# Kernel optimization log

Measured on AMD Instinct MI355X. Metric: run time of the kernel, lower is better.

Reference implementation:

```python
import jax, jax.numpy as jnp
import numpy as np

B, S, D, H = 2, 2048, 1024, 16
DK = D // H


def setup_inputs() -> dict:
    key = jax.random.key(0)
    ks = jax.random.split(key, 12)
    std = 1.0 / np.sqrt(D)
    inp = {
        "query": jax.random.normal(ks[0], (B, S, D), jnp.float32),
        "key": jax.random.normal(ks[1], (B, S, D), jnp.float32),
        "value": jax.random.normal(ks[2], (B, S, D), jnp.float32),
        # causal decoder mask [B, 1, S, S]; 0 -> masked
        "mask": jnp.broadcast_to(jnp.tril(jnp.ones((S, S), jnp.int32)), (B, 1, S, S)),
        "wq": jax.random.uniform(ks[3], (D, D), jnp.float32, -std, std),
        "bq": jax.random.uniform(ks[4], (D,), jnp.float32, -std, std),
        "wk": jax.random.uniform(ks[5], (D, D), jnp.float32, -std, std),
        "bk": jax.random.uniform(ks[6], (D,), jnp.float32, -std, std),
        "wv": jax.random.uniform(ks[7], (D, D), jnp.float32, -std, std),
        "bv": jax.random.uniform(ks[8], (D,), jnp.float32, -std, std),
        "wo": jax.random.uniform(ks[9], (D, D), jnp.float32, -std, std),
        "bo": jax.random.uniform(ks[10], (D,), jnp.float32, -std, std),
    }
    return inp


def _split_heads(x):
    b, s, _ = x.shape
    return x.reshape(b, s, H, DK).transpose(0, 2, 1, 3)  # [B,H,S,DK]


def reference(query, key, value, mask, wq, bq, wk, bk, wv, bv, wo, bo):
    # nn.Linear: y = x @ W^T + b
    q = _split_heads(query @ wq.T + bq)
    k = _split_heads(key @ wk.T + bk)
    v = _split_heads(value @ wv.T + bv)
    scores = jnp.einsum("bhqd,bhkd->bhqk", q, k) / np.sqrt(DK).astype(np.float32)
    scores = jnp.where(mask == 0, jnp.float32(-1e9), scores)
    attn = jax.nn.softmax(scores, axis=-1)
    # dropout is identity in eval mode
    out = jnp.einsum("bhqk,bhkd->bhqd", attn, v)
    out = out.transpose(0, 2, 1, 3).reshape(query.shape[0], -1, D)
    return out @ wo.T + bo
```

## Files before the change

### kernel.cpp

```cpp
#include <hip/hip_runtime.h>
#include <hip/hip_bf16.h>
#include <cstdint>
#include <cstddef>

#define B_ 2
#define S_ 2048
#define D_ 1024
#define H_ 16
#define DK_ 64

#define AS1 __attribute__((address_space(1)))
#define AS3 __attribute__((address_space(3)))

typedef __attribute__((ext_vector_type(8))) short short8;
typedef __attribute__((ext_vector_type(4))) float f32x4;
typedef __attribute__((ext_vector_type(16))) float f32x16;
typedef __attribute__((ext_vector_type(4))) unsigned short ushort4_t;

__device__ __forceinline__ unsigned short f2bf(float f) {
    union { float f; unsigned u; } x; x.f = f;
    unsigned r = x.u + 0x7fffu + ((x.u >> 16) & 1u);
    return (unsigned short)(r >> 16);
}

__device__ __forceinline__ unsigned pack_bf16(float lo, float hi_) {
    union { __hip_bfloat162 h; unsigned u; } cv;
    cv.h = __float22bfloat162_rn(make_float2(lo, hi_));
    return cv.u;
}

__device__ __forceinline__ float xor32f(float x, int hi) {
#if __has_builtin(__builtin_amdgcn_permlane32_swap)
    unsigned u = __builtin_bit_cast(unsigned, x);
    auto r = __builtin_amdgcn_permlane32_swap(u, u, false, false);
    return __builtin_bit_cast(float, hi ? r[0] : r[1]);
#else
    return __shfl_xor(x, 32);
#endif
}

__device__ __forceinline__ void swap32(unsigned a, unsigned b, unsigned& x, unsigned& y, int hi) {
#if __has_builtin(__builtin_amdgcn_permlane32_swap)
    auto r = __builtin_amdgcn_permlane32_swap(a, b, false, false);
    x = r[0]; y = r[1];
#else
    unsigned pa_ = __shfl_xor(a, 32), pb_ = __shfl_xor(b, 32);
    x = hi ? pb_ : a;
    y = hi ? b : pa_;
#endif
}

__global__ __launch_bounds__(256) void cvt_all(
    const float* __restrict__ q, const float* __restrict__ k, const float* __restrict__ v,
    const float* __restrict__ wq, const float* __restrict__ wk, const float* __restrict__ wv,
    const float* __restrict__ wo,
    unsigned short* __restrict__ xq, unsigned short* __restrict__ xk, unsigned short* __restrict__ xv,
    unsigned short* __restrict__ wqb, unsigned short* __restrict__ wkb, unsigned short* __restrict__ wvb,
    unsigned short* __restrict__ wob) {
    int b = blockIdx.x;
    const float* src; unsigned short* dst; int rel;
    if (b < 6144) {
        int which = b >> 11; rel = b & 2047;
        src = (which == 0) ? q : (which == 1) ? k : v;
        dst = (which == 0) ? xq : (which == 1) ? xk : xv;
    } else {
        int bb = b - 6144; int which = bb >> 9; rel = bb & 511;
        src = (which == 0) ? wq : (which == 1) ? wk : (which == 2) ? wv : wo;
        dst = (which == 0) ? wqb : (which == 1) ? wkb : (which == 2) ? wvb : wob;
    }
    int i = rel * 256 + threadIdx.x;
    const float4* s4 = (const float4*)src;
    float4 a = s4[2 * i], c = s4[2 * i + 1];
    short8 o;
    o[0] = (short)f2bf(a.x); o[1] = (short)f2bf(a.y); o[2] = (short)f2bf(a.z); o[3] = (short)f2bf(a.w);
    o[4] = (short)f2bf(c.x); o[5] = (short)f2bf(c.y); o[6] = (short)f2bf(c.z); o[7] = (short)f2bf(c.w);
    *(short8*)(dst + (size_t)i * 8) = o;
}

template <int OUTMODE>
__device__ __forceinline__ void gemm_body(const unsigned short* __restrict__ A,
                                          const unsigned short* __restrict__ W,
                                          const float* __restrict__ bias,
                                          void* __restrict__ Cout, float scale) {
    constexpr int Kd = 1024;
    __shared__ unsigned short As[128 * 64];
    __shared__ unsigned short Bs[128 * 64];
    const int t = threadIdx.x;
    const int l = t & 63;
    const int l15 = l & 15, l4 = l >> 4;
    const int wid = t >> 6;
    const int wm = wid >> 1, wn = wid & 1;
    const int m0 = (blockIdx.x * 4 + (blockIdx.y & 3)) * 128;
    const int n0 = (blockIdx.y >> 2) * 128;

    f32x4 acc[4][4] = {};

    int ldsoff[4];
    size_t sgoff[4];
#pragma unroll
    for (int p = 0; p < 4; p++) {
        int off = p * 4096 + t * 16;
        int row = off >> 7;
        int slot = (off >> 4) & 7;
        ldsoff[p] = off;
        sgoff[p] = (size_t)row * Kd + (size_t)((slot ^ (row & 7)) * 8);
    }

    for (int k0 = 0; k0 < Kd; k0 += 64) {
#pragma unroll
        for (int p = 0; p < 4; p++)
            __builtin_amdgcn_global_load_lds(
                (const AS1 void*)(A + (size_t)m0 * Kd + sgoff[p] + k0),
                (AS3 void*)((char*)As + ldsoff[p]), 16, 0, 0);
#pragma unroll
        for (int p = 0; p < 4; p++)
            __builtin_amdgcn_global_load_lds(
                (const AS1 void*)(W + (size_t)n0 * Kd + sgoff[p] + k0),
                (AS3 void*)((char*)Bs + ldsoff[p]), 16, 0, 0);
        __syncthreads();
#pragma unroll
        for (int kk = 0; kk < 2; kk++) {
            short8 af[4], bfr[4];
#pragma unroll
            for (int mi = 0; mi < 4; mi++) {
                int row = wm * 64 + mi * 16 + l15;
                int slot = kk * 4 + l4;
                af[mi] = *(const short8*)((const char*)As + row * 128 + ((slot ^ (row & 7)) << 4));
            }
#pragma unroll
            for (int ni = 0; ni < 4; ni++) {
                int row = wn * 64 + ni * 16 + l15;
                int slot = kk * 4 + l4;
                bfr[ni] = *(const short8*)((const char*)Bs + row * 128 + ((slot ^ (row & 7)) << 4));
            }
#pragma unroll
            for (int mi = 0; mi < 4; mi++)
#pragma unroll
                for (int ni = 0; ni < 4; ni++)
                    acc[mi][ni] = __builtin_amdgcn_mfma_f32_16x16x32_bf16(af[mi], bfr[ni], acc[mi][ni], 0, 0, 0);
        }
        __syncthreads();
    }

#pragma unroll
    for (int mi = 0; mi < 4; mi++) {
#pragma unroll
        for (int ni = 0; ni < 4; ni++) {
            int n = n0 + wn * 64 + ni * 16 + l15;
            float bn = bias[n];
            int mb = m0 + wm * 64 + mi * 16 + l4 * 4;
            if constexpr (OUTMODE == 2) {
                int b = mb >> 11, s = mb & 2047, h = n >> 6, dk = n & 63;
                ushort4_t vv;
#pragma unroll
                for (int j = 0; j < 4; j++) vv[j] = f2bf(acc[mi][ni][j] + bn);
                *(ushort4_t*)((unsigned short*)Cout + ((size_t)(b * H_ + h) * DK_ + dk) * S_ + s) = vv;
            } else {
#pragma unroll
                for (int j = 0; j < 4; j++) {
                    float v = (acc[mi][ni][j] + bn) * scale;
                    int m = mb + j;
                    if constexpr (OUTMODE == 0) {
                        int b = m >> 11, s = m & 2047, h = n >> 6, dk = n & 63;
                        ((unsigned short*)Cout)[(((size_t)b * H_ + h) * S_ + s) * DK_ + dk] = f2bf(v);
                    } else {
                        ((float*)Cout)[(size_t)m * D_ + n] = v;
                    }
                }
            }
        }
    }
}

__global__ __launch_bounds__(256) void qkv_gemm(
    const unsigned short* __restrict__ xq, const unsigned short* __restrict__ xk,
    const unsigned short* __restrict__ xv, const unsigned short* __restrict__ wqb,
    const unsigned short* __restrict__ wkb, const unsigned short* __restrict__ wvb,
    const float* __restrict__ bq, const float* __restrict__ bk, const float* __restrict__ bv,
    unsigned short* __restrict__ qo, unsigned short* __restrict__ ko, unsigned short* __restrict__ vto,
    float qscale) {
    int z = blockIdx.z;
    if (z == 2) {
        gemm_body<2>(xv, wvb, bv, vto, 1.0f);
    } else {
        const unsigned short* A = (z == 0) ? xq : xk;
        const unsigned short* W = (z == 0) ? wqb : wkb;
        const float* bias = (z == 0) ? bq : bk;
        unsigned short* out = (z == 0) ? qo : ko;
        float scale = (z == 0) ? qscale : 1.0f;
        gemm_body<0>(A, W, bias, out, scale);
    }
}

__global__ __launch_bounds__(256) void out_gemm(const unsigned short* __restrict__ Aa,
                                                const unsigned short* __restrict__ Wo,
                                                const float* __restrict__ bo,
                                                float* __restrict__ out) {
    gemm_body<1>(Aa, Wo, bo, out, 1.0f);
}

union AttnSm {
    unsigned short kv[2][2][128 * 64];
    struct { float obuf[2][2][32][64]; float lArr[2][4][32]; } m;
};

__device__ __forceinline__ void attn_compute(const short8 kf[4], const short8 vf[4],
                                             const short8 qf[4], int lq, int hi, bool diag,
                                             f32x16& o0, f32x16& o1, float& l_run) {
    f32x16 sT = {};
    __builtin_amdgcn_s_setprio(1);
#pragma unroll
    for (int c = 0; c < 4; c++)
        sT = __builtin_amdgcn_mfma_f32_32x32x16_bf16(kf[c], qf[c], sT, 0, 0, 0);
    __builtin_amdgcn_s_setprio(0);

    float e[16];
#pragma unroll
    for (int r = 0; r < 16; r++) e[r] = exp2f(sT[r]);
    if (diag) {
#pragma unroll
        for (int r = 0; r < 16; r++) {
            int kvl = (r & 3) + 8 * (r >> 2) + 4 * hi;
            e[r] = (kvl <= lq) ? e[r] : 0.0f;
        }
    }

    float s8[8];
#pragma unroll
    for (int r = 0; r < 8; r++) s8[r] = e[2 * r] + e[2 * r + 1];
#pragma unroll
    for (int r = 0; r < 4; r++) s8[r] = s8[r] + s8[r + 4];
    float ps = (s8[0] + s8[1]) + (s8[2] + s8[3]);
    ps += xor32f(ps, hi);
    l_run += ps;

    unsigned OW[8];
#pragma unroll
    for (int w = 0; w < 8; w++) OW[w] = pack_bf16(e[2 * w], e[2 * w + 1]);

    union { unsigned u[4]; short8 s; } pa0, pa1;
    swap32(OW[0], OW[2], pa0.u[0], pa0.u[2], hi);
    swap32(OW[1], OW[3], pa0.u[1], pa0.u[3], hi);
    swap32(OW[4], OW[6], pa1.u[0], pa1.u[2], hi);
    swap32(OW[5], OW[7], pa1.u[1], pa1.u[3], hi);

    __builtin_amdgcn_s_setprio(1);
    o0 = __builtin_amdgcn_mfma_f32_32x32x16_bf16(pa0.s, vf[0], o0, 0, 0, 0);
    o1 = __builtin_amdgcn_mfma_f32_32x32x16_bf16(pa0.s, vf[1], o1, 0, 0, 0);
    o0 = __builtin_amdgcn_mfma_f32_32x32x16_bf16(pa1.s, vf[2], o0, 0, 0, 0);
    o1 = __builtin_amdgcn_mfma_f32_32x32x16_bf16(pa1.s, vf[3], o1, 0, 0, 0);
    __builtin_amdgcn_s_setprio(0);
}

__global__ __launch_bounds__(512, 4) void attn_kernel(const unsigned short* __restrict__ Q,
                                                      const unsigned short* __restrict__ Kk,
                                                      const unsigned short* __restrict__ Vt,
                                                      unsigned short* __restrict__ Aout) {
    __shared__ AttnSm sm;

    const int t_ = threadIdx.x;
    const int l = t_ & 63;
    const int w = t_ >> 6;
    const int qsub = w >> 2, kvw = w & 3;
    const int lq = l & 31, hi = l >> 5;

    const int bid = blockIdx.x;
    const int xcd = bid & 7, j = bid >> 3;
    const int bh = xcd * 4 + (j >> 5);
    const int bq = 31 - (j & 31);
    const int wq0 = bq * 64;
    const int qi = 2 * bq + qsub;
    const int T = ((2 * bq + 1) >> 2) + 1;

    const unsigned short* Qh = Q + (size_t)bh * S_ * DK_;
    const unsigned short* Kh = Kk + (size_t)bh * S_ * DK_;
    const unsigned short* Vth = Vt + (size_t)bh * DK_ * S_;

    short8 qf[4];
    const unsigned short* qrow = Qh + (size_t)(wq0 + qsub * 32 + lq) * DK_ + hi * 8;
#pragma unroll
    for (int c = 0; c < 4; c++) qf[c] = *(const short8*)(qrow + 16 * c);

    f32x16 o0 = {}, o1 = {};
    float l_run = 0.f;

    const int lr = kvw * 32 + lq;
    unsigned kaddr[4], vaddr[4];
#pragma unroll
    for (int c = 0; c < 4; c++)
        kaddr[c] = (unsigned)(lr * 128 + (((2 * c + hi) ^ (lr & 7)) << 4));
#pragma unroll
    for (int c = 0; c < 2; c++) {
        unsigned sl = (unsigned)(((kvw * 4 + 2 * c + hi) ^ (lq & 15)) << 4);
        vaddr[2 * c] = (unsigned)(lq * 256) + sl;
        vaddr[2 * c + 1] = (unsigned)((lq + 32) * 256) + sl;
    }

    const int off0 = t_ * 16, off1 = 8192 + t_ * 16;
    int ldsoff[2] = {off0, off1};
    const char* kgp[2];
    const char* vgp[2];
#pragma unroll
    for (int p = 0; p < 2; p++) {
        int off = (p == 0) ? off0 : off1;
        int rk = off >> 7, slk = (off >> 4) & 7;
        kgp[p] = (const char*)Kh + rk * 128 + ((slk ^ (rk & 7)) << 4);
        int rv = off >> 8, slv = (off >> 4) & 15;
        vgp[p] = (const char*)Vth + (size_t)rv * (S_ * 2) + ((slv ^ (rv & 15)) << 4);
    }

#define STAGE(BUF)                                                                      \
    {                                                                                   \
        _Pragma("unroll") for (int p = 0; p < 2; p++) {                                 \
            __builtin_amdgcn_global_load_lds((const AS1 void*)kgp[p],                   \
                (AS3 void*)((char*)sm.kv[BUF][0] + ldsoff[p]), 16, 0, 0);               \
            kgp[p] += 128 * DK_ * 2;                          \
        }                                                                               \
        _Pragma("unroll") for (int p = 0; p < 2; p++) {                                 \
            __builtin_amdgcn_global_load_lds((const AS1 void*)vgp[p],                   \
                (AS3 void*)((char*)sm.kv[BUF][1] + ldsoff[p]), 16, 0, 0);               \
            vgp[p] += 128 * 2;                     \
        }                                                                               \
    }

#define TILE_STEP(BUF, T_IDX)                                                           \
    {                                                                                   \
        if ((T_IDX) + 1 < T) { asm volatile("s_waitcnt vmcnt(4)" ::: "memory"); }       \
        else                 { asm volatile("s_waitcnt vmcnt(0)" ::: "memory"); }       \
        __builtin_amdgcn_sched_barrier(0);                                              \
        __builtin_amdgcn_s_barrier();                                                   \
        __builtin_amdgcn_sched_barrier(0);                                              \
        const int sidx = 4 * (T_IDX) + kvw;                                             \
        if (sidx <= qi) {                                                               \
            short8 kf[4], vf[4];                                                        \
            const char* Kbuf = (const char*)sm.kv[BUF][0];                              \
            const char* Vbuf = (const char*)sm.kv[BUF][1];                              \
            _Pragma("unroll") for (int c = 0; c < 4; c++)                               \
                kf[c] = *(const short8*)(Kbuf + kaddr[c]);                              \
            _Pragma("unroll") for (int c = 0; c < 4; c++)                               \
                vf[c] = *(const short8*)(Vbuf + vaddr[c]);                              \
            attn_compute(kf, vf, qf, lq, hi, sidx == qi, o0, o1, l_run);                \
        }                                                                               \
        asm volatile("s_waitcnt lgkmcnt(0)" ::: "memory");                              \
        __builtin_amdgcn_sched_barrier(0);                                              \
        __builtin_amdgcn_s_barrier();                                                   \
        __builtin_amdgcn_sched_barrier(0);                                              \
        if ((T_IDX) + 2 < T) STAGE(BUF);                                                \
    }

    STAGE(0);
    STAGE(1);

    for (int t = 0; t < T; t += 2) {
        TILE_STEP(0, t);
        if (t + 1 < T) TILE_STEP(1, t + 1);
    }
#undef TILE_STEP
#undef STAGE

    float(&obuf)[2][2][32][64] = sm.m.obuf;
    float(&lArr)[2][4][32] = sm.m.lArr;
    if (hi == 0) lArr[qsub][kvw][lq] = l_run;

    if (kvw < 2) {
#pragma unroll
        for (int r = 0; r < 16; r++) {
            int qrw = (r & 3) + 8 * (r >> 2) + 4 * hi;
            obuf[qsub][kvw][qrw][lq] = o0[r];
            obuf[qsub][kvw][qrw][lq + 32] = o1[r];
        }
    }
    __syncthreads();
    if (kvw >= 2) {
#pragma unroll
        for (int r = 0; r < 16; r++) {
            int qrw = (r & 3) + 8 * (r >> 2) + 4 * hi;
            obuf[qsub][kvw - 2][qrw][lq] += o0[r];
            obuf[qsub][kvw - 2][qrw][lq + 32] += o1[r];
        }
    }
    __syncthreads();

    const int b = bh >> 4, h = bh & 15;
    const int row = (w & 3) * 8 + (l >> 3);
    const int dk0 = (l & 7) * 8;
    float ls = lArr[qsub][0][row] + lArr[qsub][1][row] + lArr[qsub][2][row] + lArr[qsub][3][row];
    float inv = 1.0f / ls;
    short8 ov;
#pragma unroll
    for (int jj = 0; jj < 8; jj++) {
        float s = obuf[qsub][0][row][dk0 + jj] + obuf[qsub][1][row][dk0 + jj];
        ov[jj] = (short)f2bf(s * inv);
    }
    unsigned short* orow = Aout + ((size_t)b * S_ + (wq0 + qsub * 32 + row)) * D_ + h * 64 + dk0;
    *(short8*)orow = ov;
}

extern "C" void kernel_launch(void* const* d_in, const int* in_sizes, int n_in,
                              void* d_out, int out_size, void* d_ws, size_t ws_size,
                              hipStream_t stream) {
    const float* query = (const float*)d_in[0];
    const float* key = (const float*)d_in[1];
    const float* value = (const float*)d_in[2];
    const float* wq = (const float*)d_in[4];
    const float* bq = (const float*)d_in[5];
    const float* wk = (const float*)d_in[6];
    const float* bk = (const float*)d_in[7];
    const float* wv = (const float*)d_in[8];
    const float* bv = (const float*)d_in[9];
    const float* wo = (const float*)d_in[10];
    const float* bo = (const float*)d_in[11];

    const size_t NX = (size_t)B_ * S_ * D_;
    const size_t NW = (size_t)D_ * D_;
    char* p = (char*)d_ws;
    unsigned short* xq = (unsigned short*)p; p += NX * 2;
    unsigned short* xk = (unsigned short*)p; p += NX * 2;
    unsigned short* xv = (unsigned short*)p; p += NX * 2;
    unsigned short* wqb = (unsigned short*)p; p += NW * 2;
    unsigned short* wkb = (unsigned short*)p; p += NW * 2;
    unsigned short* wvb = (unsigned short*)p; p += NW * 2;
    unsigned short* wob = (unsigned short*)p; p += NW * 2;
    unsigned short* qb = (unsigned short*)p; p += NX * 2;
    unsigned short* kb = (unsigned short*)p; p += NX * 2;
    unsigned short* vtb = (unsigned short*)p; p += NX * 2;
    unsigned short* ab = (unsigned short*)p; p += NX * 2;

    cvt_all<<<dim3(8192), dim3(256), 0, stream>>>(query, key, value, wq, wk, wv, wo,
                                                  xq, xk, xv, wqb, wkb, wvb, wob);

    const float qscale = 0.125f * 1.4426950408889634f;
    qkv_gemm<<<dim3(8, 32, 3), dim3(256), 0, stream>>>(xq, xk, xv, wqb, wkb, wvb,
                                                       bq, bk, bv, qb, kb, vtb, qscale);
    attn_kernel<<<dim3(1024), dim3(512), 0, stream>>>(qb, kb, vtb, ab);
    out_gemm<<<dim3(8, 32), dim3(256), 0, stream>>>(ab, wob, bo, (float*)d_out);
}
```

Before: 128.3 us.

## Fuse fp32-to-bf16 conversion into GEMM tile loads and drop conversion kernel

Removes the standalone conversion kernel that turned fp32 activations and weights into bf16 workspace copies. The QKV and output GEMMs now load fp32 directly from global memory into registers, convert to bf16, and store into the swizzled shared tiles. This removes a full extra read-write pass and one launch. In exchange, the GEMMs re-read fp32 data at twice the bytes per tile and lose the asynchronous direct-to-LDS loads for those operands.

After: 189.6 us. 1.48x slower.

```diff
diff --git a/kernel.cpp b/kernel.cpp
--- a/kernel.cpp
+++ b/kernel.cpp
@@ -50,36 +50,9 @@
 #endif
 }
 
-__global__ __launch_bounds__(256) void cvt_all(
-    const float* __restrict__ q, const float* __restrict__ k, const float* __restrict__ v,
-    const float* __restrict__ wq, const float* __restrict__ wk, const float* __restrict__ wv,
-    const float* __restrict__ wo,
-    unsigned short* __restrict__ xq, unsigned short* __restrict__ xk, unsigned short* __restrict__ xv,
-    unsigned short* __restrict__ wqb, unsigned short* __restrict__ wkb, unsigned short* __restrict__ wvb,
-    unsigned short* __restrict__ wob) {
-    int b = blockIdx.x;
-    const float* src; unsigned short* dst; int rel;
-    if (b < 6144) {
-        int which = b >> 11; rel = b & 2047;
-        src = (which == 0) ? q : (which == 1) ? k : v;
-        dst = (which == 0) ? xq : (which == 1) ? xk : xv;
-    } else {
-        int bb = b - 6144; int which = bb >> 9; rel = bb & 511;
-        src = (which == 0) ? wq : (which == 1) ? wk : (which == 2) ? wv : wo;
-        dst = (which == 0) ? wqb : (which == 1) ? wkb : (which == 2) ? wvb : wob;
-    }
-    int i = rel * 256 + threadIdx.x;
-    const float4* s4 = (const float4*)src;
-    float4 a = s4[2 * i], c = s4[2 * i + 1];
-    short8 o;
-    o[0] = (short)f2bf(a.x); o[1] = (short)f2bf(a.y); o[2] = (short)f2bf(a.z); o[3] = (short)f2bf(a.w);
-    o[4] = (short)f2bf(c.x); o[5] = (short)f2bf(c.y); o[6] = (short)f2bf(c.z); o[7] = (short)f2bf(c.w);
-    *(short8*)(dst + (size_t)i * 8) = o;
-}
-
-template <int OUTMODE>
-__device__ __forceinline__ void gemm_body(const unsigned short* __restrict__ A,
-                                          const unsigned short* __restrict__ W,
+template <int OUTMODE, int AF32, int WF32>
+__device__ __forceinline__ void gemm_body(const void* __restrict__ Ap,
+                                          const void* __restrict__ Wp,
                                           const float* __restrict__ bias,
                                           void* __restrict__ Cout, float scale) {
     constexpr int Kd = 1024;
@@ -93,30 +66,76 @@
     const int m0 = (blockIdx.x * 4 + (blockIdx.y & 3)) * 128;
     const int n0 = (blockIdx.y >> 2) * 128;
 
+    const unsigned short* Ab = (const unsigned short*)Ap;
+    const unsigned short* Wb = (const unsigned short*)Wp;
+    const float* Af = (const float*)Ap;
+    const float* Wf = (const float*)Wp;
+
     f32x4 acc[4][4] = {};
 
     int ldsoff[4];
-    size_t sgoff[4];
+    int sgo[4];
 #pragma unroll
     for (int p = 0; p < 4; p++) {
         int off = p * 4096 + t * 16;
         int row = off >> 7;
         int slot = (off >> 4) & 7;
         ldsoff[p] = off;
-        sgoff[p] = (size_t)row * Kd + (size_t)((slot ^ (row & 7)) * 8);
+        sgo[p] = row * Kd + (slot ^ (row & 7)) * 8;
     }
 
     for (int k0 = 0; k0 < Kd; k0 += 64) {
-#pragma unroll
-        for (int p = 0; p < 4; p++)
-            __builtin_amdgcn_global_load_lds(
-                (const AS1 void*)(A + (size_t)m0 * Kd + sgoff[p] + k0),
-                (AS3 void*)((char*)As + ldsoff[p]), 16, 0, 0);
-#pragma unroll
-        for (int p = 0; p < 4; p++)
-            __builtin_amdgcn_global_load_lds(
-                (const AS1 void*)(W + (size_t)n0 * Kd + sgoff[p] + k0),
-                (AS3 void*)((char*)Bs + ldsoff[p]), 16, 0, 0);
+        float4 av[4][2], wv[4][2];
+        if constexpr (AF32) {
+#pragma unroll
+            for (int p = 0; p < 4; p++) {
+                const float* s = Af + (size_t)m0 * Kd + sgo[p] + k0;
+                av[p][0] = *(const float4*)(s);
+                av[p][1] = *(const float4*)(s + 4);
+            }
+        } else {
+#pragma unroll
+            for (int p = 0; p < 4; p++)
+                __builtin_amdgcn_global_load_lds(
+                    (const AS1 void*)(Ab + (size_t)m0 * Kd + sgo[p] + k0),
+                    (AS3 void*)((char*)As + ldsoff[p]), 16, 0, 0);
+        }
+        if constexpr (WF32) {
+#pragma unroll
+            for (int p = 0; p < 4; p++) {
+                const float* s = Wf + (size_t)n0 * Kd + sgo[p] + k0;
+                wv[p][0] = *(const float4*)(s);
+                wv[p][1] = *(const float4*)(s + 4);
+            }
+        } else {
+#pragma unroll
+            for (int p = 0; p < 4; p++)
+                __builtin_amdgcn_global_load_lds(
+                    (const AS1 void*)(Wb + (size_t)n0 * Kd + sgo[p] + k0),
+                    (AS3 void*)((char*)Bs + ldsoff[p]), 16, 0, 0);
+        }
+        if constexpr (AF32) {
+#pragma unroll
+            for (int p = 0; p < 4; p++) {
+                short8 o;
+                o[0] = (short)f2bf(av[p][0].x); o[1] = (short)f2bf(av[p][0].y);
+                o[2] = (short)f2bf(av[p][0].z); o[3] = (short)f2bf(av[p][0].w);
+                o[4] = (short)f2bf(av[p][1].x); o[5] = (short)f2bf(av[p][1].y);
+                o[6] = (short)f2bf(av[p][1].z); o[7] = (short)f2bf(av[p][1].w);
+                *(short8*)((char*)As + ldsoff[p]) = o;
+            }
+        }
+        if constexpr (WF32) {
+#pragma unroll
+            for (int p = 0; p < 4; p++) {
+                short8 o;
+                o[0] = (short)f2bf(wv[p][0].x); o[1] = (short)f2bf(wv[p][0].y);
+                o[2] = (short)f2bf(wv[p][0].z); o[3] = (short)f2bf(wv[p][0].w);
+                o[4] = (short)f2bf(wv[p][1].x); o[5] = (short)f2bf(wv[p][1].y);
+                o[6] = (short)f2bf(wv[p][1].z); o[7] = (short)f2bf(wv[p][1].w);
+                *(short8*)((char*)Bs + ldsoff[p]) = o;
+            }
+        }
         __syncthreads();
 #pragma unroll
         for (int kk = 0; kk < 2; kk++) {
@@ -173,30 +192,26 @@
 }
 
 __global__ __launch_bounds__(256) void qkv_gemm(
-    const unsigned short* __restrict__ xq, const unsigned short* __restrict__ xk,
-    const unsigned short* __restrict__ xv, const unsigned short* __restrict__ wqb,
-    const unsigned short* __restrict__ wkb, const unsigned short* __restrict__ wvb,
+    const float* __restrict__ q, const float* __restrict__ k, const float* __restrict__ v,
+    const float* __restrict__ wq, const float* __restrict__ wk, const float* __restrict__ wv,
     const float* __restrict__ bq, const float* __restrict__ bk, const float* __restrict__ bv,
     unsigned short* __restrict__ qo, unsigned short* __restrict__ ko, unsigned short* __restrict__ vto,
     float qscale) {
     int z = blockIdx.z;
     if (z == 2) {
-        gemm_body<2>(xv, wvb, bv, vto, 1.0f);
+        gemm_body<2, 1, 1>(v, wv, bv, vto, 1.0f);
+    } else if (z == 0) {
+        gemm_body<0, 1, 1>(q, wq, bq, qo, qscale);
     } else {
-        const unsigned short* A = (z == 0) ? xq : xk;
-        const unsigned short* W = (z == 0) ? wqb : wkb;
-        const float* bias = (z == 0) ? bq : bk;
-        unsigned short* out = (z == 0) ? qo : ko;
-        float scale = (z == 0) ? qscale : 1.0f;
-        gemm_body<0>(A, W, bias, out, scale);
+        gemm_body<0, 1, 1>(k, wk, bk, ko, 1.0f);
     }
 }
 
 __global__ __launch_bounds__(256) void out_gemm(const unsigned short* __restrict__ Aa,
-                                                const unsigned short* __restrict__ Wo,
+                                                const float* __restrict__ Wo,
                                                 const float* __restrict__ bo,
                                                 float* __restrict__ out) {
-    gemm_body<1>(Aa, Wo, bo, out, 1.0f);
+    gemm_body<1, 0, 1>(Aa, Wo, bo, out, 1.0f);
 }
 
 union AttnSm {
@@ -412,26 +427,15 @@
     const float* bo = (const float*)d_in[11];
 
     const size_t NX = (size_t)B_ * S_ * D_;
-    const size_t NW = (size_t)D_ * D_;
     char* p = (char*)d_ws;
-    unsigned short* xq = (unsigned short*)p; p += NX * 2;
-    unsigned short* xk = (unsigned short*)p; p += NX * 2;
-    unsigned short* xv = (unsigned short*)p; p += NX * 2;
-    unsigned short* wqb = (unsigned short*)p; p += NW * 2;
-    unsigned short* wkb = (unsigned short*)p; p += NW * 2;
-    unsigned short* wvb = (unsigned short*)p; p += NW * 2;
-    unsigned short* wob = (unsigned short*)p; p += NW * 2;
     unsigned short* qb = (unsigned short*)p; p += NX * 2;
     unsigned short* kb = (unsigned short*)p; p += NX * 2;
     unsigned short* vtb = (unsigned short*)p; p += NX * 2;
     unsigned short* ab = (unsigned short*)p; p += NX * 2;
 
-    cvt_all<<<dim3(8192), dim3(256), 0, stream>>>(query, key, value, wq, wk, wv, wo,
-                                                  xq, xk, xv, wqb, wkb, wvb, wob);
-
     const float qscale = 0.125f * 1.4426950408889634f;
-    qkv_gemm<<<dim3(8, 32, 3), dim3(256), 0, stream>>>(xq, xk, xv, wqb, wkb, wvb,
+    qkv_gemm<<<dim3(8, 32, 3), dim3(256), 0, stream>>>(query, key, value, wq, wk, wv,
                                                        bq, bk, bv, qb, kb, vtb, qscale);
     attn_kernel<<<dim3(1024), dim3(512), 0, stream>>>(qb, kb, vtb, ab);
-    out_gemm<<<dim3(8, 32), dim3(256), 0, stream>>>(ab, wob, bo, (float*)d_out);
-}
+    out_gemm<<<dim3(8, 32), dim3(256), 0, stream>>>(ab, wo, bo, (float*)d_out);
+}
```
